# Optimization experiments

Hardware: AMD Instinct MI355X
Metric: run time of the kernel (lower is better)

The kernel has to match this reference:

```python
import jax, jax.numpy as jnp
import numpy as np
from jax import lax

TOP_K = 6
N_EXPERTS = 160
N_GROUP = 8
TOPK_GROUP = 3
ROUTED_SCALING = 16.0
AUX_ALPHA = 0.001
HIDDEN = 2048
BSZ, SEQ = 4, 4096


def setup_inputs() -> dict:
    key = jax.random.key(0)
    k1, k2 = jax.random.split(key)
    hidden_states = jax.random.normal(k1, (BSZ, SEQ, HIDDEN), dtype=jnp.float32)
    # kaiming-uniform-ish init for the gate kernel (n_experts, hidden)
    limit = float(np.sqrt(6.0 / HIDDEN))
    kernel = jax.random.uniform(k2, (N_EXPERTS, HIDDEN), dtype=jnp.float32,
                                minval=-limit, maxval=limit)
    return {"hidden_states": hidden_states, "kernel": kernel}


def reference(hidden_states, kernel):
    bsz, seq_len, h = hidden_states.shape
    x = hidden_states.reshape(-1, h).astype(jnp.float32)          # [T, h]
    logits = jnp.einsum("th,eh->te", x, kernel.astype(jnp.float32))  # [T, E]
    scores = jax.nn.softmax(logits, axis=-1)

    # group-limited greedy top-k
    experts_per_group = N_EXPERTS // N_GROUP
    group_scores = scores.reshape(-1, N_GROUP, experts_per_group).max(axis=-1)  # [T, G]
    top_group_idx = lax.top_k(group_scores, TOPK_GROUP)[1]                      # [T, Kg]
    rows = jnp.arange(group_scores.shape[0])[:, None]
    group_mask = jnp.zeros_like(group_scores).at[rows, top_group_idx].set(1.0)  # [T, G]
    score_mask = jnp.repeat(group_mask[:, :, None], experts_per_group, axis=2)
    score_mask = score_mask.reshape(-1, N_EXPERTS)                              # [T, E]
    masked_scores = jnp.where(score_mask > 0, scores, 0.0)
    topk_weight, topk_idx = lax.top_k(masked_scores, TOP_K)                     # [T, K]

    # norm_topk_prob = False -> scale by routed_scaling_factor
    topk_weight = topk_weight * ROUTED_SCALING

    # aux loss (seq_aux = False branch)
    mask_ce = jax.nn.one_hot(topk_idx.reshape(-1), num_classes=N_EXPERTS,
                             dtype=jnp.float32)                                 # [T*K, E]
    ce = jnp.mean(mask_ce, axis=0)                                              # [E]
    Pi = jnp.mean(scores, axis=0)                                               # [E]
    fi = ce * N_EXPERTS
    aux_loss = jnp.sum(Pi * fi) * AUX_ALPHA

    return topk_idx, topk_weight, aux_loss
```

## Files before the change

### kernel.cpp

```cpp
#include <hip/hip_runtime.h>
#include <math.h>


#define T_TOKENS 16384
#define HID      2048
#define NEXP     160
#define NGRP     8
#define EPG      20
#define KGRP     3
#define KTOP     6

#define BT     256
#define NKQ    4
#define KQLEN  512
#define NBODY  16
#define ABY    32768
#define BBY    20480
#define BUF    53248
#define NEPI   256
#define LPAD   68
#define PSTR   (256 * 160 * 64)

typedef __attribute__((ext_vector_type(8))) short short8;
typedef __attribute__((ext_vector_type(4))) float f32x4;
typedef __attribute__((ext_vector_type(4))) unsigned int uint4v;

union U4S8 { uint4v u; short8 s; float4 f; };

__device__ __forceinline__ unsigned short f2bf(float f) {
    unsigned u = __float_as_uint(f);
    return (unsigned short)((u + 0x7FFFu + ((u >> 16) & 1u)) >> 16);
}
__device__ __forceinline__ float bf2f(unsigned short s) {
    return __uint_as_float(((unsigned)s) << 16);
}
__device__ __forceinline__ unsigned cvtpk(float a, float b) {
    unsigned r;
    asm volatile("v_cvt_pk_bf16_f32 %0, %1, %2" : "=v"(r) : "v"(a), "v"(b));
    return r;
}
__device__ __forceinline__ float lo16(unsigned u) { return __uint_as_float(u << 16); }
__device__ __forceinline__ float hi16(unsigned u) { return __uint_as_float(u & 0xFFFF0000u); }

__device__ __forceinline__ void cp16(char* lds, const float* g) {
    __builtin_amdgcn_global_load_lds(
        (const __attribute__((address_space(1))) unsigned int*)g,
        (__attribute__((address_space(3))) unsigned int*)lds, 16, 0, 0);
}

__global__ __launch_bounds__(256)
void pack_w(const float* __restrict__ W, short* __restrict__ wpk)
{
    const int idx = blockIdx.x * 256 + threadIdx.x;
    const int e  = idx >> 8;
    const int kc = idx & 255;
    const int k0 = kc * 8;
    const float* src = W + (size_t)e * HID + k0;
    float x[8];
    *(float4*)&x[0] = *(const float4*)src;
    *(float4*)&x[4] = *(const float4*)(src + 4);
    short8 h, l;
#pragma unroll
    for (int j = 0; j < 8; ++j) {
        unsigned short hb = f2bf(x[j]);
        h[j] = (short)hb;
        l[j] = (short)f2bf(x[j] - bf2f(hb));
    }
    const int s    = kc >> 2;
    const int kg   = kc & 3;
    const int lane = kg * 16 + (e & 15);
    const int nt   = e >> 4;
    const size_t base = (size_t)((s * 10 + nt) * 2) * 1024 + (size_t)lane * 16;
    *(short8*)((char*)wpk + base)        = h;
    *(short8*)((char*)wpk + base + 1024) = l;
}

__global__ __launch_bounds__(512, 1)
void moe_gemm(const float* __restrict__ X, const short* __restrict__ wpk,
              float* __restrict__ glog)
{
    __shared__ __align__(16) char smem[2 * BUF];

    const int tid  = threadIdx.x;
    const int lane = tid & 63;
    const int wave = tid >> 6;
    const int tokgrp = wave >> 1;
    const int ns     = wave & 1;
    const int tb = blockIdx.x >> 2;
    const int kq = blockIdx.x & 3;
    const int tokBase = tb * BT;
    const char* wpkB = (const char*)wpk + (size_t)(kq * NBODY) * BBY;

    const float* srcA[4];
#pragma unroll
    for (int j = 0; j < 4; ++j) {
        const int idx = tid + j * 512;
        const int r = idx >> 3, c = idx & 7;
        srcA[j] = X + (size_t)(tokBase + r) * HID + kq * KQLEN + ((c ^ (r & 7)) << 2);
    }

    const int lr = lane & 15;
    const int kg = lane >> 4;
    const int c0s = (((kg * 2    ) ^ (lr & 7)) << 4);
    const int c1s = (((kg * 2 + 1) ^ (lr & 7)) << 4);
    int rbase[4];
#pragma unroll
    for (int mt = 0; mt < 4; ++mt) rbase[mt] = (tokgrp * 64 + mt * 16 + lr) * 128;
    const int boff = ABY + ns * 10240 + lane * 16;

    f32x4 acc[4][5];
#pragma unroll
    for (int m = 0; m < 4; ++m)
#pragma unroll
        for (int n = 0; n < 5; ++n) acc[m][n] = (f32x4){0.f, 0.f, 0.f, 0.f};

#define STG(BI, S) { char* b_ = smem + (BI) * BUF;                               \
    _Pragma("unroll") for (int j = 0; j < 4; ++j)                                \
        cp16(b_ + (tid + j * 512) * 16, srcA[j] + (S) * 32);                     \
    cp16(b_ + ABY + tid * 16,                                                    \
         (const float*)(wpkB + (size_t)(S) * BBY + tid * 16));                   \
    cp16(b_ + ABY + (tid + 512) * 16,                                            \
         (const float*)(wpkB + (size_t)(S) * BBY + (tid + 512) * 16));           \
    if (tid < 256)                                                               \
        cp16(b_ + ABY + (tid + 1024) * 16,                                       \
             (const float*)(wpkB + (size_t)(S) * BBY + (tid + 1024) * 16)); }

    STG(0, 0)
    __syncthreads();

#pragma unroll 1
    for (int s = 0; s < NBODY; ++s) {
        if (s < NBODY - 1) STG((s + 1) & 1, s + 1)
        const char* ab = smem + (s & 1) * BUF;

#pragma unroll
        for (int mt = 0; mt < 4; ++mt) {
            U4S8 af0, af1, ah, al;
            af0.f = *(const float4*)(ab + rbase[mt] + c0s);
            af1.f = *(const float4*)(ab + rbase[mt] + c1s);
            unsigned ph0 = cvtpk(af0.f.x, af0.f.y), ph1 = cvtpk(af0.f.z, af0.f.w);
            unsigned ph2 = cvtpk(af1.f.x, af1.f.y), ph3 = cvtpk(af1.f.z, af1.f.w);
            float l0 = af0.f.x - lo16(ph0), l1 = af0.f.y - hi16(ph0);
            float l2 = af0.f.z - lo16(ph1), l3 = af0.f.w - hi16(ph1);
            float l4 = af1.f.x - lo16(ph2), l5 = af1.f.y - hi16(ph2);
            float l6 = af1.f.z - lo16(ph3), l7 = af1.f.w - hi16(ph3);
            ah.u[0] = ph0; ah.u[1] = ph1; ah.u[2] = ph2; ah.u[3] = ph3;
            al.u[0] = cvtpk(l0, l1); al.u[1] = cvtpk(l2, l3);
            al.u[2] = cvtpk(l4, l5); al.u[3] = cvtpk(l6, l7);

#pragma unroll
            for (int nt = 0; nt < 5; ++nt) {
                U4S8 bh, bl;
                bh.u = *(const uint4v*)(ab + boff + nt * 2048);
                bl.u = *(const uint4v*)(ab + boff + nt * 2048 + 1024);
                acc[mt][nt] = __builtin_amdgcn_mfma_f32_16x16x32_bf16(ah.s, bh.s, acc[mt][nt], 0, 0, 0);
                acc[mt][nt] = __builtin_amdgcn_mfma_f32_16x16x32_bf16(ah.s, bl.s, acc[mt][nt], 0, 0, 0);
                acc[mt][nt] = __builtin_amdgcn_mfma_f32_16x16x32_bf16(al.s, bh.s, acc[mt][nt], 0, 0, 0);
            }
        }
        __syncthreads();
    }
#undef STG

    float* gb = glog + ((size_t)kq * 256 + tb * 4 + tokgrp) * (NEXP * 64);
#pragma unroll
    for (int mt = 0; mt < 4; ++mt)
#pragma unroll
    for (int nt = 0; nt < 5; ++nt) {
        const int e = ns * 80 + nt * 16 + lr;
        *(f32x4*)(gb + e * 64 + mt * 16 + kg * 4) = acc[mt][nt];
    }
}

__global__ __launch_bounds__(512, 2)
void moe_epi(const float* __restrict__ glog, float* __restrict__ out,
             float* __restrict__ piPart, unsigned int* __restrict__ histPart,
             unsigned int* __restrict__ flagCnt, unsigned int* __restrict__ flagList)
{
    __shared__ __align__(16) float pL[NEXP * LPAD];
    __shared__ __align__(16) float m_arr[64];
    __shared__ __align__(16) float invd_arr[64];
    __shared__ unsigned histL[NEXP];

    const int tid  = threadIdx.x;
    const int lane = tid & 63;
    const int tokBase = blockIdx.x * 64;
    const float* gb = glog + (size_t)blockIdx.x * (NEXP * 64);

#pragma unroll
    for (int j = 0; j < 5; ++j) {
        const int i = tid + j * 512;
        const int e = i >> 4, t4 = (i & 15) << 2;
        const float* p = gb + e * 64 + t4;
        float4 v0 = *(const float4*)(p);
        float4 v1 = *(const float4*)(p + PSTR);
        float4 v2 = *(const float4*)(p + 2 * (size_t)PSTR);
        float4 v3 = *(const float4*)(p + 3 * (size_t)PSTR);
        float4 v;
        v.x = (v0.x + v1.x) + (v2.x + v3.x);
        v.y = (v0.y + v1.y) + (v2.y + v3.y);
        v.z = (v0.z + v1.z) + (v2.z + v3.z);
        v.w = (v0.w + v1.w) + (v2.w + v3.w);
        *(float4*)&pL[e * LPAD + t4] = v;
    }
    if (tid < NEXP) histL[tid] = 0;
    __syncthreads();

    {
        const int t  = tid >> 3;
        const int gl = tid & 7;
        const int lbase = lane & 0x38;

        float mg_ = pL[(gl * EPG) * LPAD + t];
#pragma unroll
        for (int j = 1; j < EPG; ++j) mg_ = fmaxf(mg_, pL[(gl * EPG + j) * LPAD + t]);

        float gv[8];
#pragma unroll
        for (int gi = 0; gi < 8; ++gi) gv[gi] = __shfl(mg_, lbase + gi);

        float best = -1e30f; int bi = 0;
#pragma unroll
        for (int gi = 0; gi < NGRP; ++gi) if (gv[gi] > best) { best = gv[gi]; bi = gi; }
        const int sel0 = bi; int gmask = 1 << bi;
        best = -1e30f; bi = 0;
#pragma unroll
        for (int gi = 0; gi < NGRP; ++gi)
            if (!((gmask >> gi) & 1) && gv[gi] > best) { best = gv[gi]; bi = gi; }
        const int sel1 = bi; gmask |= 1 << bi;
        best = -1e30f; bi = 0;
#pragma unroll
        for (int gi = 0; gi < NGRP; ++gi)
            if (!((gmask >> gi) & 1) && gv[gi] > best) { best = gv[gi]; bi = gi; }
        const int sel2 = bi; gmask |= 1 << bi;
        const float g3v = best;
        float g4v = -1e30f;
#pragma unroll
        for (int gi = 0; gi < NGRP; ++gi)
            if (!((gmask >> gi) & 1)) g4v = fmaxf(g4v, gv[gi]);
        float mall = gv[0];
#pragma unroll
        for (int gi = 1; gi < NGRP; ++gi) mall = fmaxf(mall, gv[gi]);

        float dsum = 0.f;
#pragma unroll
        for (int j = 0; j < EPG; ++j)
            dsum += expf(pL[(gl * EPG + j) * LPAD + t] - mall);
        dsum += __shfl_xor(dsum, 1);
        dsum += __shfl_xor(dsum, 2);
        dsum += __shfl_xor(dsum, 4);
        const float invd = 1.0f / dsum;

        float cvv[8]; int ce[8];
#pragma unroll
        for (int c = 0; c < 8; ++c) {
            const int i = gl + 8 * c;
            if (i < 60) {
                const int sgrp = (i >= 40) ? sel2 : ((i >= 20) ? sel1 : sel0);
                const int e = sgrp * EPG + (i - ((i >= 40) ? 40 : ((i >= 20) ? 20 : 0)));
                ce[c] = e;
                cvv[c] = pL[e * LPAD + t];
            } else { ce[c] = 999; cvv[c] = -1e30f; }
        }

        int ch0, ch1, ch2, ch3, ch4, ch5;
        float cv0, cv1, cv2, cv3, cv4, cv5, cv6;
#pragma unroll
        for (int p = 0; p < 7; ++p) {
            float bv = -1e30f; int be = 999;
#pragma unroll
            for (int c = 0; c < 8; ++c)
                if (cvv[c] > bv || (cvv[c] == bv && ce[c] < be)) { bv = cvv[c]; be = ce[c]; }
#pragma unroll
            for (int off = 1; off < 8; off <<= 1) {
                const float ov = __shfl_xor(bv, off);
                const int   oe = __shfl_xor(be, off);
                if (ov > bv || (ov == bv && oe < be)) { bv = ov; be = oe; }
            }
#pragma unroll
            for (int c = 0; c < 8; ++c) if (ce[c] == be) cvv[c] = -1e30f;
            if (p == 0) { ch0 = be; cv0 = bv; }
            else if (p == 1) { ch1 = be; cv1 = bv; }
            else if (p == 2) { ch2 = be; cv2 = bv; }
            else if (p == 3) { ch3 = be; cv3 = bv; }
            else if (p == 4) { ch4 = be; cv4 = bv; }
            else if (p == 5) { ch5 = be; cv5 = bv; }
            else { cv6 = bv; }
        }

        if (gl == 0) {
            const int gt = tokBase + t;
            out[(size_t)gt * KTOP + 0] = (float)ch0;
            out[(size_t)gt * KTOP + 1] = (float)ch1;
            out[(size_t)gt * KTOP + 2] = (float)ch2;
            out[(size_t)gt * KTOP + 3] = (float)ch3;
            out[(size_t)gt * KTOP + 4] = (float)ch4;
            out[(size_t)gt * KTOP + 5] = (float)ch5;
            float* wo = out + (size_t)T_TOKENS * KTOP + (size_t)gt * KTOP;
            wo[0] = expf(cv0 - mall) * invd * 16.0f;
            wo[1] = expf(cv1 - mall) * invd * 16.0f;
            wo[2] = expf(cv2 - mall) * invd * 16.0f;
            wo[3] = expf(cv3 - mall) * invd * 16.0f;
            wo[4] = expf(cv4 - mall) * invd * 16.0f;
            wo[5] = expf(cv5 - mall) * invd * 16.0f;
            atomicAdd(&histL[ch0], 1u); atomicAdd(&histL[ch1], 1u);
            atomicAdd(&histL[ch2], 1u); atomicAdd(&histL[ch3], 1u);
            atomicAdd(&histL[ch4], 1u); atomicAdd(&histL[ch5], 1u);
            m_arr[t] = mall; invd_arr[t] = invd;
            float mg2 = g3v - g4v;
            mg2 = fminf(mg2, cv0 - cv1); mg2 = fminf(mg2, cv1 - cv2);
            mg2 = fminf(mg2, cv2 - cv3); mg2 = fminf(mg2, cv3 - cv4);
            mg2 = fminf(mg2, cv4 - cv5); mg2 = fminf(mg2, cv5 - cv6);
            if (mg2 < 1e-4f) {
                const unsigned pos = atomicAdd(flagCnt, 1u);
                flagList[pos] = (unsigned)gt;
            }
        }
    }
    __syncthreads();

    if (tid < NEXP) {
        const float* Le = pL + tid * LPAD;
        float s = 0.f;
#pragma unroll 4
        for (int t0 = 0; t0 < 64; t0 += 4) {
            const float4 lv = *(const float4*)(Le + t0);
            const float4 mv = *(const float4*)(m_arr + t0);
            const float4 iv = *(const float4*)(invd_arr + t0);
            s += expf(lv.x - mv.x) * iv.x;
            s += expf(lv.y - mv.y) * iv.y;
            s += expf(lv.z - mv.z) * iv.z;
            s += expf(lv.w - mv.w) * iv.w;
        }
        piPart[(size_t)tid * NEPI + blockIdx.x]   = s;
        histPart[(size_t)tid * NEPI + blockIdx.x] = histL[tid];
    }
}

__global__ __launch_bounds__(1024)
void moe_gate_fixup(const float* __restrict__ X, const float* __restrict__ W,
                    float* __restrict__ out, const unsigned int* __restrict__ flagCnt,
                    const unsigned int* __restrict__ flagList)
{
    __shared__ float xs[HID];
    __shared__ double ld[NEXP];
    const int nflag = (int)*flagCnt;
    const int tid = threadIdx.x;
    const int wv = tid >> 6, ln = tid & 63;

    for (int i = blockIdx.x; i < nflag; i += gridDim.x) {
        const int t = (int)flagList[i];
        __syncthreads();
        for (int k = tid; k < HID / 4; k += 1024)
            ((float4*)xs)[k] = ((const float4*)(X + (size_t)t * HID))[k];
        __syncthreads();

#pragma unroll 1
        for (int e = wv; e < NEXP; e += 16) {
            const float* wr = W + (size_t)e * HID + ln * 4;
            const float* xp = xs + ln * 4;
            float4 w4[8];
#pragma unroll
            for (int j = 0; j < 8; ++j) w4[j] = *(const float4*)(wr + j * 256);
            double a0 = 0.0, a1 = 0.0;
#pragma unroll
            for (int j = 0; j < 8; ++j) {
                a0 = fma((double)xp[j * 256 + 0], (double)w4[j].x, a0);
                a1 = fma((double)xp[j * 256 + 1], (double)w4[j].y, a1);
                a0 = fma((double)xp[j * 256 + 2], (double)w4[j].z, a0);
                a1 = fma((double)xp[j * 256 + 3], (double)w4[j].w, a1);
            }
            double a = a0 + a1;
#pragma unroll
            for (int off = 32; off > 0; off >>= 1) a += __shfl_down(a, off);
            if (ln == 0) ld[e] = a;
        }
        __syncthreads();

        if (wv == 0) {
            const int gl = ln & 7;
            const int lbase = ln & 0x38;

            double gm = ld[gl * EPG];
#pragma unroll
            for (int j = 1; j < EPG; ++j) {
                const double v = ld[gl * EPG + j];
                if (v > gm) gm = v;
            }
            double gv[8];
#pragma unroll
            for (int gi = 0; gi < 8; ++gi) gv[gi] = __shfl(gm, lbase + gi);

            double best = -1.0e300; int bi = 0;
#pragma unroll
            for (int gi = 0; gi < NGRP; ++gi)
                if (gv[gi] > best) { best = gv[gi]; bi = gi; }
            const int sel0 = bi; int gmask = 1 << bi;
            best = -1.0e300; bi = 0;
#pragma unroll
            for (int gi = 0; gi < NGRP; ++gi)
                if (!((gmask >> gi) & 1) && gv[gi] > best) { best = gv[gi]; bi = gi; }
            const int sel1 = bi; gmask |= 1 << bi;
            best = -1.0e300; bi = 0;
#pragma unroll
            for (int gi = 0; gi < NGRP; ++gi)
                if (!((gmask >> gi) & 1) && gv[gi] > best) { best = gv[gi]; bi = gi; }
            const int sel2 = bi; gmask |= 1 << bi;
            double mall = gv[0];
#pragma unroll
            for (int gi = 1; gi < NGRP; ++gi) if (gv[gi] > mall) mall = gv[gi];

            float dsum = 0.f;
#pragma unroll
            for (int j = 0; j < EPG; ++j)
                dsum += expf((float)(ld[gl * EPG + j] - mall));
            dsum += __shfl_xor(dsum, 1);
            dsum += __shfl_xor(dsum, 2);
            dsum += __shfl_xor(dsum, 4);
            const float invd = 1.0f / dsum;

            double cvv[8]; int ce[8];
#pragma unroll
            for (int c = 0; c < 8; ++c) {
                const int idx = gl + 8 * c;
                if (idx < 60) {
                    const int sgrp = (idx >= 40) ? sel2 : ((idx >= 20) ? sel1 : sel0);
                    const int e = sgrp * EPG + (idx - ((idx >= 40) ? 40 : ((idx >= 20) ? 20 : 0)));
                    ce[c] = e;
                    cvv[c] = ld[e];
                } else { ce[c] = 999; cvv[c] = -1.0e300; }
            }

#pragma unroll
            for (int p = 0; p < KTOP; ++p) {
                double bv = -1.0e300; int be = 999;
#pragma unroll
                for (int c = 0; c < 8; ++c)
                    if (cvv[c] > bv || (cvv[c] == bv && ce[c] < be)) { bv = cvv[c]; be = ce[c]; }
#pragma unroll
                for (int off = 1; off < 8; off <<= 1) {
                    const double ov = __shfl_xor(bv, off);
                    const int    oe = __shfl_xor(be, off);
                    if (ov > bv || (ov == bv && oe < be)) { bv = ov; be = oe; }
                }
#pragma unroll
                for (int c = 0; c < 8; ++c) if (ce[c] == be) cvv[c] = -1.0e300;
                if (ln == 0) {
                    out[(size_t)t * KTOP + p] = (float)be;
                    out[(size_t)T_TOKENS * KTOP + (size_t)t * KTOP + p] =
                        expf((float)(bv - mall)) * invd * 16.0f;
                }
            }
        }
        __syncthreads();
    }
}

__global__ __launch_bounds__(256)
void moe_gate_aux(const float* __restrict__ piPart,
                  const unsigned int* __restrict__ histPart,
                  float* __restrict__ out)
{
    __shared__ double buf[NEXP];
    const int tid = threadIdx.x;
    if (tid < NEXP) {
        const float* pp = piPart + (size_t)tid * NEPI;
        const unsigned int* hp = histPart + (size_t)tid * NEPI;
        float s = 0.f;
        unsigned c = 0;
#pragma unroll 8
        for (int b = 0; b < NEPI; ++b) { s += pp[b]; c += hp[b]; }
        buf[tid] = (double)s * (double)c;
    }
    __syncthreads();
    if (tid == 0) {
        double s = 0.0;
        for (int e = 0; e < NEXP; ++e) s += buf[e];
        const double aux = s * (0.001 * (double)NEXP) /
                           ((double)T_TOKENS * (double)T_TOKENS * (double)KTOP);
        out[(size_t)T_TOKENS * KTOP * 2] = (float)aux;
    }
}

extern "C" void kernel_launch(void* const* d_in, const int* in_sizes, int n_in,
                              void* d_out, int out_size, void* d_ws, size_t ws_size,
                              hipStream_t stream)
{
    const float* X = (const float*)d_in[0];
    const float* W = (const float*)d_in[1];
    float* out = (float*)d_out;

    char* ws = (char*)d_ws;
    short* wpk = (short*)ws;
    float* glog = (float*)(ws + 1310720);
    float* piPart = (float*)(ws + 43253760);
    unsigned int* histPart = (unsigned int*)(ws + 43417600);
    unsigned int* flagCnt  = (unsigned int*)(ws + 43581440);
    unsigned int* flagList = (unsigned int*)(ws + 43581456);

    hipMemsetAsync(flagCnt, 0, 16, stream);
    pack_w<<<160, 256, 0, stream>>>(W, wpk);
    moe_gemm<<<256, 512, 0, stream>>>(X, wpk, glog);
    moe_epi<<<NEPI, 512, 0, stream>>>(glog, out, piPart, histPart, flagCnt, flagList);
    moe_gate_fixup<<<512, 1024, 0, stream>>>(X, W, out, flagCnt, flagList);
    moe_gate_aux<<<1, 256, 0, stream>>>(piPart, histPart, out);
}
```

Baseline: 112.0 us.

## Halve GEMM token tile, read weights directly from global, fold flag reset into pack

Halves the GEMM block token tile from 256 to 128 and doubles the grid to 512 blocks. Weight fragments are now loaded straight from global memory into registers each k-step instead of being staged through LDS, which cuts LDS to 32 KB so up to 4 blocks per CU can run. The glog partial layout and the epilogue indexing change to match the 32-token tiles. The flag-counter memset is folded into pack_w, dropping one launch. The risks are more redundant weight traffic from global/L2 and lower per-block MFMA reuse.

```diff
diff --git a/kernel.cpp b/kernel.cpp
--- a/kernel.cpp
+++ b/kernel.cpp
@@ -10,16 +10,14 @@
 #define KGRP     3
 #define KTOP     6
 
-#define BT     256
+#define BT     128
 #define NKQ    4
 #define KQLEN  512
 #define NBODY  16
-#define ABY    32768
-#define BBY    20480
-#define BUF    53248
+#define ABY    16384
 #define NEPI   256
 #define LPAD   68
-#define PSTR   (256 * 160 * 64)
+#define PSTR   (512 * 160 * 32)
 
 typedef __attribute__((ext_vector_type(8))) short short8;
 typedef __attribute__((ext_vector_type(4))) float f32x4;
@@ -49,8 +47,10 @@
 }
 
 __global__ __launch_bounds__(256)
-void pack_w(const float* __restrict__ W, short* __restrict__ wpk)
+void pack_w(const float* __restrict__ W, short* __restrict__ wpk,
+            unsigned int* __restrict__ flagCnt)
 {
+    if (blockIdx.x == 0 && threadIdx.x == 0) flagCnt[0] = 0;
     const int idx = blockIdx.x * 256 + threadIdx.x;
     const int e  = idx >> 8;
     const int kc = idx & 255;
@@ -75,11 +75,11 @@
     *(short8*)((char*)wpk + base + 1024) = l;
 }
 
-__global__ __launch_bounds__(512, 1)
+__global__ __launch_bounds__(512, 4)
 void moe_gemm(const float* __restrict__ X, const short* __restrict__ wpk,
               float* __restrict__ glog)
 {
-    __shared__ __align__(16) char smem[2 * BUF];
+    __shared__ __align__(16) char smem[2 * ABY];
 
     const int tid  = threadIdx.x;
     const int lane = tid & 63;
@@ -89,11 +89,10 @@
     const int tb = blockIdx.x >> 2;
     const int kq = blockIdx.x & 3;
     const int tokBase = tb * BT;
-    const char* wpkB = (const char*)wpk + (size_t)(kq * NBODY) * BBY;
-
-    const float* srcA[4];
-#pragma unroll
-    for (int j = 0; j < 4; ++j) {
+
+    const float* srcA[2];
+#pragma unroll
+    for (int j = 0; j < 2; ++j) {
         const int idx = tid + j * 512;
         const int r = idx >> 3, c = idx & 7;
         srcA[j] = X + (size_t)(tokBase + r) * HID + kq * KQLEN + ((c ^ (r & 7)) << 2);
@@ -103,41 +102,42 @@
     const int kg = lane >> 4;
     const int c0s = (((kg * 2    ) ^ (lr & 7)) << 4);
     const int c1s = (((kg * 2 + 1) ^ (lr & 7)) << 4);
-    int rbase[4];
-#pragma unroll
-    for (int mt = 0; mt < 4; ++mt) rbase[mt] = (tokgrp * 64 + mt * 16 + lr) * 128;
-    const int boff = ABY + ns * 10240 + lane * 16;
-
-    f32x4 acc[4][5];
-#pragma unroll
-    for (int m = 0; m < 4; ++m)
+    int rb[2];
+#pragma unroll
+    for (int mt = 0; mt < 2; ++mt) rb[mt] = (tokgrp * 32 + mt * 16 + lr) * 128;
+    const char* wb = (const char*)wpk
+                   + ((size_t)(kq * NBODY) * 10 + ns * 5) * 2048 + (size_t)lane * 16;
+
+    f32x4 acc[2][5];
+#pragma unroll
+    for (int m = 0; m < 2; ++m)
 #pragma unroll
         for (int n = 0; n < 5; ++n) acc[m][n] = (f32x4){0.f, 0.f, 0.f, 0.f};
 
-#define STG(BI, S) { char* b_ = smem + (BI) * BUF;                               \
-    _Pragma("unroll") for (int j = 0; j < 4; ++j)                                \
-        cp16(b_ + (tid + j * 512) * 16, srcA[j] + (S) * 32);                     \
-    cp16(b_ + ABY + tid * 16,                                                    \
-         (const float*)(wpkB + (size_t)(S) * BBY + tid * 16));                   \
-    cp16(b_ + ABY + (tid + 512) * 16,                                            \
-         (const float*)(wpkB + (size_t)(S) * BBY + (tid + 512) * 16));           \
-    if (tid < 256)                                                               \
-        cp16(b_ + ABY + (tid + 1024) * 16,                                       \
-             (const float*)(wpkB + (size_t)(S) * BBY + (tid + 1024) * 16)); }
-
-    STG(0, 0)
+#define STGA(BI, S) { char* b_ = smem + (BI) * ABY;                          \
+    cp16(b_ + tid * 16,         srcA[0] + (S) * 32);                         \
+    cp16(b_ + (tid + 512) * 16, srcA[1] + (S) * 32); }
+
+    STGA(0, 0)
     __syncthreads();
 
 #pragma unroll 1
     for (int s = 0; s < NBODY; ++s) {
-        if (s < NBODY - 1) STG((s + 1) & 1, s + 1)
-        const char* ab = smem + (s & 1) * BUF;
-
-#pragma unroll
-        for (int mt = 0; mt < 4; ++mt) {
+        U4S8 bh[5], bl[5];
+        const char* wbs = wb + (size_t)s * 20480;
+#pragma unroll
+        for (int nt = 0; nt < 5; ++nt) {
+            bh[nt].u = *(const uint4v*)(wbs + nt * 2048);
+            bl[nt].u = *(const uint4v*)(wbs + nt * 2048 + 1024);
+        }
+        if (s < NBODY - 1) STGA((s + 1) & 1, s + 1)
+
+        const char* ab = smem + (s & 1) * ABY;
+#pragma unroll
+        for (int mt = 0; mt < 2; ++mt) {
             U4S8 af0, af1, ah, al;
-            af0.f = *(const float4*)(ab + rbase[mt] + c0s);
-            af1.f = *(const float4*)(ab + rbase[mt] + c1s);
+            af0.f = *(const float4*)(ab + rb[mt] + c0s);
+            af1.f = *(const float4*)(ab + rb[mt] + c1s);
             unsigned ph0 = cvtpk(af0.f.x, af0.f.y), ph1 = cvtpk(af0.f.z, af0.f.w);
             unsigned ph2 = cvtpk(af1.f.x, af1.f.y), ph3 = cvtpk(af1.f.z, af1.f.w);
             float l0 = af0.f.x - lo16(ph0), l1 = af0.f.y - hi16(ph0);
@@ -150,25 +150,22 @@
 
 #pragma unroll
             for (int nt = 0; nt < 5; ++nt) {
-                U4S8 bh, bl;
-                bh.u = *(const uint4v*)(ab + boff + nt * 2048);
-                bl.u = *(const uint4v*)(ab + boff + nt * 2048 + 1024);
-                acc[mt][nt] = __builtin_amdgcn_mfma_f32_16x16x32_bf16(ah.s, bh.s, acc[mt][nt], 0, 0, 0);
-                acc[mt][nt] = __builtin_amdgcn_mfma_f32_16x16x32_bf16(ah.s, bl.s, acc[mt][nt], 0, 0, 0);
-                acc[mt][nt] = __builtin_amdgcn_mfma_f32_16x16x32_bf16(al.s, bh.s, acc[mt][nt], 0, 0, 0);
+                acc[mt][nt] = __builtin_amdgcn_mfma_f32_16x16x32_bf16(ah.s, bh[nt].s, acc[mt][nt], 0, 0, 0);
+                acc[mt][nt] = __builtin_amdgcn_mfma_f32_16x16x32_bf16(ah.s, bl[nt].s, acc[mt][nt], 0, 0, 0);
+                acc[mt][nt] = __builtin_amdgcn_mfma_f32_16x16x32_bf16(al.s, bh[nt].s, acc[mt][nt], 0, 0, 0);
             }
         }
         __syncthreads();
     }
-#undef STG
-
-    float* gb = glog + ((size_t)kq * 256 + tb * 4 + tokgrp) * (NEXP * 64);
-#pragma unroll
-    for (int mt = 0; mt < 4; ++mt)
+#undef STGA
+
+    float* gb = glog + (size_t)kq * PSTR + (size_t)(tb * 4 + tokgrp) * (NEXP * 32);
+#pragma unroll
+    for (int mt = 0; mt < 2; ++mt)
 #pragma unroll
     for (int nt = 0; nt < 5; ++nt) {
         const int e = ns * 80 + nt * 16 + lr;
-        *(f32x4*)(gb + e * 64 + mt * 16 + kg * 4) = acc[mt][nt];
+        *(f32x4*)(gb + e * 32 + mt * 16 + kg * 4) = acc[mt][nt];
     }
 }
 
@@ -185,13 +182,15 @@
     const int tid  = threadIdx.x;
     const int lane = tid & 63;
     const int tokBase = blockIdx.x * 64;
-    const float* gb = glog + (size_t)blockIdx.x * (NEXP * 64);
 
 #pragma unroll
     for (int j = 0; j < 5; ++j) {
         const int i = tid + j * 512;
-        const int e = i >> 4, t4 = (i & 15) << 2;
-        const float* p = gb + e * 64 + t4;
+        const int e = i >> 4;
+        const int q = (i & 15) << 2;
+        const int tt = 2 * blockIdx.x + (q >> 5);
+        const int off = q & 31;
+        const float* p = glog + (size_t)tt * (NEXP * 32) + e * 32 + off;
         float4 v0 = *(const float4*)(p);
         float4 v1 = *(const float4*)(p + PSTR);
         float4 v2 = *(const float4*)(p + 2 * (size_t)PSTR);
@@ -201,7 +200,7 @@
         v.y = (v0.y + v1.y) + (v2.y + v3.y);
         v.z = (v0.z + v1.z) + (v2.z + v3.z);
         v.w = (v0.w + v1.w) + (v2.w + v3.w);
-        *(float4*)&pL[e * LPAD + t4] = v;
+        *(float4*)&pL[e * LPAD + q] = v;
     }
     if (tid < NEXP) histL[tid] = 0;
     __syncthreads();
@@ -498,9 +497,8 @@
     unsigned int* flagCnt  = (unsigned int*)(ws + 43581440);
     unsigned int* flagList = (unsigned int*)(ws + 43581456);
 
-    hipMemsetAsync(flagCnt, 0, 16, stream);
-    pack_w<<<160, 256, 0, stream>>>(W, wpk);
-    moe_gemm<<<256, 512, 0, stream>>>(X, wpk, glog);
+    pack_w<<<160, 256, 0, stream>>>(W, wpk, flagCnt);
+    moe_gemm<<<512, 512, 0, stream>>>(X, wpk, glog);
     moe_epi<<<NEPI, 512, 0, stream>>>(glog, out, piPart, histPart, flagCnt, flagList);
     moe_gate_fixup<<<512, 1024, 0, stream>>>(X, W, out, flagCnt, flagList);
     moe_gate_aux<<<1, 256, 0, stream>>>(piPart, histPart, out);
```

Measured after the change: 105.2 us. 6.1% less time.
